# Kernel tuning notes

Hardware: AMD Instinct MI355X
Metric: run time of the kernel (lower is better)

Reference implementation:

```python
import jax, jax.numpy as jnp
import numpy as np

K = 2          # neighbors per point (init default k=2)
ALPHA = 5e-4   # regularization weight (init default)
N_CLASSES = 1000


def setup_inputs() -> dict:
    key = jax.random.key(0)
    k1, k2, k3 = jax.random.split(key, 3)
    n, d_feat, n_cls = 4096, 1024, N_CLASSES
    x_batch = jax.random.normal(k1, (n, d_feat), dtype=jnp.float32)
    y_batch = jax.random.randint(k2, (n,), 0, n_cls, dtype=jnp.int32)
    y_output = jax.random.normal(k3, (n, n_cls), dtype=jnp.float32)
    return {"x_batch": x_batch, "y_batch": y_batch, "y_output": y_output}


def _pairwise_dist(a):
    # ||a_i - a_j|| via gram trick; clamp for numerical safety.
    sq = jnp.sum(a * a, axis=-1)                       # [n]
    d2 = sq[:, None] + sq[None, :] - 2.0 * (a @ a.T)   # [n, n]
    d2 = jnp.maximum(d2, 0.0)
    # sqrt with zero-safe gradient (diag / coincident points)
    safe = jnp.where(d2 > 0.0, d2, 1.0)
    return jnp.where(d2 > 0.0, jnp.sqrt(safe), 0.0)


def reference(x_batch, y_batch, y_output):
    n = x_batch.shape[0]
    d = _pairwise_dist(x_batch)                        # [n, n] input-space distances

    # K nearest neighbors, excluding self (i != j in the original loops)
    d_knn = d + jnp.where(jnp.eye(n, dtype=bool), jnp.inf, 0.0)
    _, nbr_idx = jax.lax.top_k(-d_knn, K)              # [n, K] smallest distances
    nbr_mask = jnp.zeros((n, n), dtype=d.dtype)
    nbr_mask = nbr_mask.at[jnp.arange(n)[:, None], nbr_idx].set(1.0)

    same_class = (y_batch[:, None] == y_batch[None, :])
    w = jnp.exp(-d) * nbr_mask                         # exp(-d) on KNN edges only
    # w_diff = w_int - w_pen: +exp(-d) for same-class neighbors, -exp(-d) otherwise
    w_diff = jnp.where(same_class, w, -w)

    y_norm = _pairwise_dist(y_output)                  # [n, n] ||y_out_i - y_out_j||
    reg_value = jnp.sum(w_diff * y_norm)
    return ALPHA * reg_value
```

## Files before the change

kernel.cpp:

```cpp
#include <hip/hip_runtime.h>
#include <math.h>

#define ALPHA 5e-4f
#define BIG 1e30f

typedef __attribute__((ext_vector_type(8))) short bf16x8;
typedef __attribute__((ext_vector_type(4))) float f32x4;

__device__ __forceinline__ unsigned short f2bf(float x) {
    unsigned u = __builtin_bit_cast(unsigned, x);
    unsigned r = (u + 0x7FFFu + ((u >> 16) & 1u)) >> 16;
    return (unsigned short)r;
}
__device__ __forceinline__ float bf2f(unsigned short b) {
    unsigned u = ((unsigned)b) << 16;
    return __builtin_bit_cast(float, u);
}

__device__ __forceinline__ void gload16(const short* g, short* l) {
    __builtin_amdgcn_global_load_lds(
        (const __attribute__((address_space(1))) void*)g,
        (__attribute__((address_space(3))) void*)l, 16, 0, 0);
}

__global__ __launch_bounds__(256)
void conv_rownorm_kernel(const float* __restrict__ X, short* __restrict__ Xb,
                         float* __restrict__ sqn, int d) {
    const int w = threadIdx.x >> 6, lane = threadIdx.x & 63;
    const int row = blockIdx.x * 4 + w;
    const float4* src = reinterpret_cast<const float4*>(X + (size_t)row * d);
    short4* dst = reinterpret_cast<short4*>(Xb + (size_t)row * d);
    float s = 0.f;
    const int nv = d >> 2;
    for (int c = lane; c < nv; c += 64) {
        float4 v = src[c];
        unsigned short b0 = f2bf(v.x), b1 = f2bf(v.y), b2 = f2bf(v.z), b3 = f2bf(v.w);
        float x0 = bf2f(b0), x1 = bf2f(b1), x2 = bf2f(b2), x3 = bf2f(b3);
        s += x0 * x0 + x1 * x1 + x2 * x2 + x3 * x3;
        dst[c] = make_short4((short)b0, (short)b1, (short)b2, (short)b3);
    }
    for (int off = 1; off < 64; off <<= 1) s += __shfl_xor(s, off, 64);
    if (lane == 0) sqn[row] = s;
}

#define BM 128
#define BN 128
#define BK 32

__global__ __launch_bounds__(256)
void gram_top2_mfma(const short* __restrict__ Xb, const float* __restrict__ sqn,
                    float* __restrict__ cand_s, int* __restrict__ cand_i,
                    int n, int d, int nb) {
    __shared__ short As[2][BM * BK];
    __shared__ short Bs[2][BN * BK];

    int rb = 0, rem = blockIdx.x;
    while (rem >= nb - rb) { rem -= nb - rb; ++rb; }
    const int cb = rb + rem;

    const int row0 = rb * BM, col0 = cb * BN;
    const int t = threadIdx.x;
    const int w = t >> 6, l = t & 63;
    const int wr = w >> 1, wc = w & 1;
    const int lc = l & 15, lg = l >> 4;

    f32x4 acc[4][4];
#pragma unroll
    for (int i = 0; i < 4; ++i)
#pragma unroll
        for (int j = 0; j < 4; ++j) acc[i][j] = (f32x4){0.f, 0.f, 0.f, 0.f};

    const int gchunk = (t & 3) ^ ((t >> 3) & 3);
    const size_t gA0 = (size_t)(row0 + (t >> 2)) * d + gchunk * 8;
    const size_t gB0 = (size_t)(col0 + (t >> 2)) * d + gchunk * 8;
    const size_t rstep = (size_t)64 * d;

    const int kswz = (lg ^ ((lc >> 1) & 3)) * 8;

    {
        short* la = As[0] + w * 512;
        short* lb = Bs[0] + w * 512;
        gload16(Xb + gA0, la);
        gload16(Xb + gA0 + rstep, la + 2048);
        gload16(Xb + gB0, lb);
        gload16(Xb + gB0 + rstep, lb + 2048);
    }
    __syncthreads();

    int cur = 0;
    for (int k0 = 0; k0 < d; k0 += BK) {
        if (k0 + BK < d) {
            short* la = As[cur ^ 1] + w * 512;
            short* lb = Bs[cur ^ 1] + w * 512;
            gload16(Xb + gA0 + k0 + BK, la);
            gload16(Xb + gA0 + k0 + BK + rstep, la + 2048);
            gload16(Xb + gB0 + k0 + BK, lb);
            gload16(Xb + gB0 + k0 + BK + rstep, lb + 2048);
        }
        bf16x8 a[4], b[4];
#pragma unroll
        for (int mi = 0; mi < 4; ++mi)
            a[mi] = *reinterpret_cast<const bf16x8*>(&As[cur][(wr * 64 + mi * 16 + lc) * BK + kswz]);
#pragma unroll
        for (int ni = 0; ni < 4; ++ni)
            b[ni] = *reinterpret_cast<const bf16x8*>(&Bs[cur][(wc * 64 + ni * 16 + lc) * BK + kswz]);
#pragma unroll
        for (int mi = 0; mi < 4; ++mi)
#pragma unroll
            for (int ni = 0; ni < 4; ++ni)
                acc[mi][ni] = __builtin_amdgcn_mfma_f32_16x16x32_bf16(
                    a[mi], b[ni], acc[mi][ni], 0, 0, 0);
        __syncthreads();
        cur ^= 1;
    }

    float sq_c[4];
#pragma unroll
    for (int ni = 0; ni < 4; ++ni) sq_c[ni] = sqn[col0 + wc * 64 + ni * 16 + lc];
    const int strip_r = cb * 2 + wc;

#pragma unroll
    for (int mi = 0; mi < 4; ++mi) {
#pragma unroll
        for (int j = 0; j < 4; ++j) {
            const int grow = row0 + wr * 64 + mi * 16 + lg * 4 + j;
            float s1 = BIG, s2 = BIG;
            int i1 = -1, i2 = -1;
#pragma unroll
            for (int ni = 0; ni < 4; ++ni) {
                const int gcol = col0 + wc * 64 + ni * 16 + lc;
                float s = sq_c[ni] - 2.f * acc[mi][ni][j];
                if (gcol == grow) s = BIG;
                if (s < s1) { s2 = s1; i2 = i1; s1 = s; i1 = gcol; }
                else if (s < s2) { s2 = s; i2 = gcol; }
            }
            for (int off = 1; off < 16; off <<= 1) {
                float b1 = __shfl_xor(s1, off, 16);
                int  bi1 = __shfl_xor(i1, off, 16);
                float b2 = __shfl_xor(s2, off, 16);
                int  bi2 = __shfl_xor(i2, off, 16);
                if (b1 < s1) { s2 = s1; i2 = i1; s1 = b1; i1 = bi1; }
                else if (b1 < s2) { s2 = b1; i2 = bi1; }
                if (b2 < s2) { s2 = b2; i2 = bi2; }
            }
            if (lc == 0) {
                size_t base = ((size_t)grow * 64 + strip_r) * 2;
                cand_s[base] = s1; cand_s[base + 1] = s2;
                cand_i[base] = i1; cand_i[base + 1] = i2;
            }
        }
    }

    if (rb != cb) {
        float sq_r[4][4];
#pragma unroll
        for (int mi = 0; mi < 4; ++mi)
#pragma unroll
            for (int j = 0; j < 4; ++j)
                sq_r[mi][j] = sqn[row0 + wr * 64 + mi * 16 + lg * 4 + j];
        const int strip_c = rb * 2 + wr;

#pragma unroll
        for (int ni = 0; ni < 4; ++ni) {
            const int gcol = col0 + wc * 64 + ni * 16 + lc;
            float s1 = BIG, s2 = BIG;
            int i1 = -1, i2 = -1;
#pragma unroll
            for (int mi = 0; mi < 4; ++mi)
#pragma unroll
                for (int j = 0; j < 4; ++j) {
                    const int grow = row0 + wr * 64 + mi * 16 + lg * 4 + j;
                    float s = sq_r[mi][j] - 2.f * acc[mi][ni][j];
                    if (s < s1) { s2 = s1; i2 = i1; s1 = s; i1 = grow; }
                    else if (s < s2) { s2 = s; i2 = grow; }
                }
#pragma unroll
            for (int off = 16; off < 64; off <<= 1) {
                float b1 = __shfl_xor(s1, off, 64);
                int  bi1 = __shfl_xor(i1, off, 64);
                float b2 = __shfl_xor(s2, off, 64);
                int  bi2 = __shfl_xor(i2, off, 64);
                if (b1 < s1) { s2 = s1; i2 = i1; s1 = b1; i1 = bi1; }
                else if (b1 < s2) { s2 = b1; i2 = bi1; }
                if (b2 < s2) { s2 = b2; i2 = bi2; }
            }
            if (lg == 0) {
                size_t base = ((size_t)gcol * 64 + strip_c) * 2;
                cand_s[base] = s1; cand_s[base + 1] = s2;
                cand_i[base] = i1; cand_i[base + 1] = i2;
            }
        }
    }
}

__global__ __launch_bounds__(256)
void merge_edges_kernel(const float* __restrict__ sqn,
                        const float* __restrict__ cand_s, const int* __restrict__ cand_i,
                        const int* __restrict__ yb, const float* __restrict__ yo,
                        float* __restrict__ partial, int ncls) {
    const int w = threadIdx.x >> 6, lane = threadIdx.x & 63;
    const int row = blockIdx.x * 4 + w;

    float2 cs = reinterpret_cast<const float2*>(cand_s + (size_t)row * 128)[lane];
    int2   ci = reinterpret_cast<const int2*>(cand_i + (size_t)row * 128)[lane];
    float s1 = cs.x, s2 = cs.y;
    int i1 = ci.x, i2 = ci.y;
    if (s2 < s1) { float ts = s1; s1 = s2; s2 = ts; int ti = i1; i1 = i2; i2 = ti; }

    for (int off = 1; off < 64; off <<= 1) {
        float b1 = __shfl_xor(s1, off, 64);
        int  bi1 = __shfl_xor(i1, off, 64);
        float b2 = __shfl_xor(s2, off, 64);
        int  bi2 = __shfl_xor(i2, off, 64);
        if (b1 < s1) { s2 = s1; i2 = i1; s1 = b1; i1 = bi1; }
        else if (b1 < s2) { s2 = b1; i2 = bi1; }
        if (b2 < s2) { s2 = b2; i2 = bi2; }
    }
    const int yr = yb[row];
    const float sr = sqn[row];
    float w1 = ((yr == yb[i1]) ? 1.f : -1.f) * expf(-sqrtf(fmaxf(sr + s1, 0.f)));
    float w2 = ((yr == yb[i2]) ? 1.f : -1.f) * expf(-sqrtf(fmaxf(sr + s2, 0.f)));

    const float4* yr4 = reinterpret_cast<const float4*>(yo + (size_t)row * ncls);
    const float4* y14 = reinterpret_cast<const float4*>(yo + (size_t)i1 * ncls);
    const float4* y24 = reinterpret_cast<const float4*>(yo + (size_t)i2 * ncls);
    const int nv4 = ncls >> 2;
    float a1 = 0.f, a2 = 0.f;
    for (int c = lane; c < nv4; c += 64) {
        float4 v = yr4[c];
        float4 u1 = y14[c];
        float4 u2 = y24[c];
        float tx = v.x - u1.x, ty = v.y - u1.y, tz = v.z - u1.z, tw = v.w - u1.w;
        a1 = fmaf(tx, tx, fmaf(ty, ty, fmaf(tz, tz, fmaf(tw, tw, a1))));
        tx = v.x - u2.x; ty = v.y - u2.y; tz = v.z - u2.z; tw = v.w - u2.w;
        a2 = fmaf(tx, tx, fmaf(ty, ty, fmaf(tz, tz, fmaf(tw, tw, a2))));
    }
    for (int c = (nv4 << 2) + lane; c < ncls; c += 64) {
        float v = yo[(size_t)row * ncls + c];
        float t1 = v - yo[(size_t)i1 * ncls + c];
        float t2 = v - yo[(size_t)i2 * ncls + c];
        a1 = fmaf(t1, t1, a1);
        a2 = fmaf(t2, t2, a2);
    }
    for (int off = 1; off < 64; off <<= 1) {
        a1 += __shfl_xor(a1, off, 64);
        a2 += __shfl_xor(a2, off, 64);
    }
    if (lane == 0)
        partial[row] = w1 * sqrtf(a1) + w2 * sqrtf(a2);
}

__global__ __launch_bounds__(256)
void final_reduce_kernel(const float* __restrict__ partial, float* __restrict__ out, int n) {
    const int t = threadIdx.x;
    __shared__ float red[4];
    float s = 0.f;
    const int nv4 = n >> 2;
    const float4* p4 = reinterpret_cast<const float4*>(partial);
    for (int c = t; c < nv4; c += 256) {
        float4 v = p4[c];
        s += v.x + v.y + v.z + v.w;
    }
    for (int off = 1; off < 64; off <<= 1) s += __shfl_xor(s, off, 64);
    if ((t & 63) == 0) red[t >> 6] = s;
    __syncthreads();
    if (t == 0) out[0] = ALPHA * (red[0] + red[1] + red[2] + red[3]);
}

extern "C" void kernel_launch(void* const* d_in, const int* in_sizes, int n_in,
                              void* d_out, int out_size, void* d_ws, size_t ws_size,
                              hipStream_t stream) {
    const float* X  = (const float*)d_in[0];
    const int*   yb = (const int*)d_in[1];
    const float* yo = (const float*)d_in[2];
    float* out = (float*)d_out;

    const int n    = in_sizes[1];
    const int d    = in_sizes[0] / n;
    const int ncls = in_sizes[2] / n;
    const int nb   = n / BM;

    char* wsb = (char*)d_ws;
    size_t off = 0;
    float* sqn = (float*)(wsb + off);    off += ((size_t)n * 4 + 255) & ~(size_t)255;
    short* Xb  = (short*)(wsb + off);    off += ((size_t)n * d * 2 + 255) & ~(size_t)255;
    float* cand_s = (float*)(wsb + off); off += ((size_t)n * 64 * 2 * 4 + 255) & ~(size_t)255;
    int*   cand_i = (int*)(wsb + off);   off += ((size_t)n * 64 * 2 * 4 + 255) & ~(size_t)255;
    float* partial = (float*)(wsb + off);

    conv_rownorm_kernel<<<n / 4, 256, 0, stream>>>(X, Xb, sqn, d);

    const int ntri = nb * (nb + 1) / 2;
    gram_top2_mfma<<<ntri, 256, 0, stream>>>(Xb, sqn, cand_s, cand_i, n, d, nb);

    merge_edges_kernel<<<n / 4, 256, 0, stream>>>(sqn, cand_s, cand_i, yb, yo, partial, ncls);

    final_reduce_kernel<<<1, 256, 0, stream>>>(partial, out, n);
}
```

Before: 60.80 us.

## Triple-buffer the gram GEMM pipeline and swizzle tiles across XCDs

```diff
diff --git a/kernel.cpp b/kernel.cpp
--- a/kernel.cpp
+++ b/kernel.cpp
@@ -50,11 +50,15 @@
 __global__ __launch_bounds__(256)
 void gram_top2_mfma(const short* __restrict__ Xb, const float* __restrict__ sqn,
                     float* __restrict__ cand_s, int* __restrict__ cand_i,
-                    int n, int d, int nb) {
-    __shared__ short As[2][BM * BK];
-    __shared__ short Bs[2][BN * BK];
-
-    int rb = 0, rem = blockIdx.x;
+                    int n, int d, int nb, int cpx) {
+    __shared__ short As[3][BM * BK];
+    __shared__ short Bs[3][BN * BK];
+
+    const int nwg = nb * (nb + 1) / 2;
+    int bid = blockIdx.x;
+    int swz = (bid & 7) * cpx + (bid >> 3);
+    (void)nwg;
+    int rb = 0, rem = swz;
     while (rem >= nb - rb) { rem -= nb - rb; ++rb; }
     const int cb = rb + rem;
 
@@ -74,44 +78,52 @@
     const size_t gA0 = (size_t)(row0 + (t >> 2)) * d + gchunk * 8;
     const size_t gB0 = (size_t)(col0 + (t >> 2)) * d + gchunk * 8;
     const size_t rstep = (size_t)64 * d;
-
     const int kswz = (lg ^ ((lc >> 1) & 3)) * 8;
+    const int wbase = w * 512;
+
+    const int nsteps = d / BK;
 
     {
-        short* la = As[0] + w * 512;
-        short* lb = Bs[0] + w * 512;
-        gload16(Xb + gA0, la);
-        gload16(Xb + gA0 + rstep, la + 2048);
-        gload16(Xb + gB0, lb);
-        gload16(Xb + gB0 + rstep, lb + 2048);
-    }
-    __syncthreads();
-
-    int cur = 0;
-    for (int k0 = 0; k0 < d; k0 += BK) {
-        if (k0 + BK < d) {
-            short* la = As[cur ^ 1] + w * 512;
-            short* lb = Bs[cur ^ 1] + w * 512;
-            gload16(Xb + gA0 + k0 + BK, la);
-            gload16(Xb + gA0 + k0 + BK + rstep, la + 2048);
-            gload16(Xb + gB0 + k0 + BK, lb);
-            gload16(Xb + gB0 + k0 + BK + rstep, lb + 2048);
+        short* la = As[0] + wbase;  short* lb = Bs[0] + wbase;
+        gload16(Xb + gA0, la);          gload16(Xb + gA0 + rstep, la + 2048);
+        gload16(Xb + gB0, lb);          gload16(Xb + gB0 + rstep, lb + 2048);
+        la = As[1] + wbase;  lb = Bs[1] + wbase;
+        gload16(Xb + gA0 + BK, la);     gload16(Xb + gA0 + BK + rstep, la + 2048);
+        gload16(Xb + gB0 + BK, lb);     gload16(Xb + gB0 + BK + rstep, lb + 2048);
+    }
+
+    int s0 = 0, s1 = 1, s2 = 2;
+    for (int ks = 0; ks < nsteps; ++ks) {
+        if (ks + 2 < nsteps) {
+            short* la = As[s2] + wbase;  short* lb = Bs[s2] + wbase;
+            const size_t ko = (size_t)(ks + 2) * BK;
+            gload16(Xb + gA0 + ko, la);      gload16(Xb + gA0 + ko + rstep, la + 2048);
+            gload16(Xb + gB0 + ko, lb);      gload16(Xb + gB0 + ko + rstep, lb + 2048);
+            asm volatile("s_waitcnt vmcnt(8)" ::: "memory");
+        } else if (ks + 1 < nsteps) {
+            asm volatile("s_waitcnt vmcnt(4)" ::: "memory");
+        } else {
+            asm volatile("s_waitcnt vmcnt(0)" ::: "memory");
         }
+        __builtin_amdgcn_s_barrier();
+
         bf16x8 a[4], b[4];
 #pragma unroll
         for (int mi = 0; mi < 4; ++mi)
-            a[mi] = *reinterpret_cast<const bf16x8*>(&As[cur][(wr * 64 + mi * 16 + lc) * BK + kswz]);
+            a[mi] = *reinterpret_cast<const bf16x8*>(&As[s0][(wr * 64 + mi * 16 + lc) * BK + kswz]);
 #pragma unroll
         for (int ni = 0; ni < 4; ++ni)
-            b[ni] = *reinterpret_cast<const bf16x8*>(&Bs[cur][(wc * 64 + ni * 16 + lc) * BK + kswz]);
+            b[ni] = *reinterpret_cast<const bf16x8*>(&Bs[s0][(wc * 64 + ni * 16 + lc) * BK + kswz]);
 #pragma unroll
         for (int mi = 0; mi < 4; ++mi)
 #pragma unroll
             for (int ni = 0; ni < 4; ++ni)
                 acc[mi][ni] = __builtin_amdgcn_mfma_f32_16x16x32_bf16(
                     a[mi], b[ni], acc[mi][ni], 0, 0, 0);
-        __syncthreads();
-        cur ^= 1;
+
+        asm volatile("s_waitcnt lgkmcnt(0)" ::: "memory");
+        __builtin_amdgcn_s_barrier();
+        int tmp = s0; s0 = s1; s1 = s2; s2 = tmp;
     }
 
     float sq_c[4];
@@ -124,28 +136,28 @@
 #pragma unroll
         for (int j = 0; j < 4; ++j) {
             const int grow = row0 + wr * 64 + mi * 16 + lg * 4 + j;
-            float s1 = BIG, s2 = BIG;
+            float s1v = BIG, s2v = BIG;
             int i1 = -1, i2 = -1;
 #pragma unroll
             for (int ni = 0; ni < 4; ++ni) {
                 const int gcol = col0 + wc * 64 + ni * 16 + lc;
                 float s = sq_c[ni] - 2.f * acc[mi][ni][j];
                 if (gcol == grow) s = BIG;
-                if (s < s1) { s2 = s1; i2 = i1; s1 = s; i1 = gcol; }
-                else if (s < s2) { s2 = s; i2 = gcol; }
+                if (s < s1v) { s2v = s1v; i2 = i1; s1v = s; i1 = gcol; }
+                else if (s < s2v) { s2v = s; i2 = gcol; }
             }
             for (int off = 1; off < 16; off <<= 1) {
-                float b1 = __shfl_xor(s1, off, 16);
+                float b1 = __shfl_xor(s1v, off, 16);
                 int  bi1 = __shfl_xor(i1, off, 16);
-                float b2 = __shfl_xor(s2, off, 16);
+                float b2 = __shfl_xor(s2v, off, 16);
                 int  bi2 = __shfl_xor(i2, off, 16);
-                if (b1 < s1) { s2 = s1; i2 = i1; s1 = b1; i1 = bi1; }
-                else if (b1 < s2) { s2 = b1; i2 = bi1; }
-                if (b2 < s2) { s2 = b2; i2 = bi2; }
+                if (b1 < s1v) { s2v = s1v; i2 = i1; s1v = b1; i1 = bi1; }
+                else if (b1 < s2v) { s2v = b1; i2 = bi1; }
+                if (b2 < s2v) { s2v = b2; i2 = bi2; }
             }
             if (lc == 0) {
                 size_t base = ((size_t)grow * 64 + strip_r) * 2;
-                cand_s[base] = s1; cand_s[base + 1] = s2;
+                cand_s[base] = s1v; cand_s[base + 1] = s2v;
                 cand_i[base] = i1; cand_i[base + 1] = i2;
             }
         }
@@ -163,7 +175,7 @@
 #pragma unroll
         for (int ni = 0; ni < 4; ++ni) {
             const int gcol = col0 + wc * 64 + ni * 16 + lc;
-            float s1 = BIG, s2 = BIG;
+            float s1v = BIG, s2v = BIG;
             int i1 = -1, i2 = -1;
 #pragma unroll
             for (int mi = 0; mi < 4; ++mi)
@@ -171,22 +183,22 @@
                 for (int j = 0; j < 4; ++j) {
                     const int grow = row0 + wr * 64 + mi * 16 + lg * 4 + j;
                     float s = sq_r[mi][j] - 2.f * acc[mi][ni][j];
-                    if (s < s1) { s2 = s1; i2 = i1; s1 = s; i1 = grow; }
-                    else if (s < s2) { s2 = s; i2 = grow; }
+                    if (s < s1v) { s2v = s1v; i2 = i1; s1v = s; i1 = grow; }
+                    else if (s < s2v) { s2v = s; i2 = grow; }
                 }
 #pragma unroll
             for (int off = 16; off < 64; off <<= 1) {
-                float b1 = __shfl_xor(s1, off, 64);
+                float b1 = __shfl_xor(s1v, off, 64);
                 int  bi1 = __shfl_xor(i1, off, 64);
-                float b2 = __shfl_xor(s2, off, 64);
+                float b2 = __shfl_xor(s2v, off, 64);
                 int  bi2 = __shfl_xor(i2, off, 64);
-                if (b1 < s1) { s2 = s1; i2 = i1; s1 = b1; i1 = bi1; }
-                else if (b1 < s2) { s2 = b1; i2 = bi1; }
-                if (b2 < s2) { s2 = b2; i2 = bi2; }
+                if (b1 < s1v) { s2v = s1v; i2 = i1; s1v = b1; i1 = bi1; }
+                else if (b1 < s2v) { s2v = b1; i2 = bi1; }
+                if (b2 < s2v) { s2v = b2; i2 = bi2; }
             }
             if (lg == 0) {
                 size_t base = ((size_t)gcol * 64 + strip_c) * 2;
-                cand_s[base] = s1; cand_s[base + 1] = s2;
+                cand_s[base] = s1v; cand_s[base + 1] = s2v;
                 cand_i[base] = i1; cand_i[base + 1] = i2;
             }
         }
@@ -291,7 +303,8 @@
     conv_rownorm_kernel<<<n / 4, 256, 0, stream>>>(X, Xb, sqn, d);
 
     const int ntri = nb * (nb + 1) / 2;
-    gram_top2_mfma<<<ntri, 256, 0, stream>>>(Xb, sqn, cand_s, cand_i, n, d, nb);
+    const int cpx  = ntri / 8;
+    gram_top2_mfma<<<ntri, 256, 0, stream>>>(Xb, sqn, cand_s, cand_i, n, d, nb, cpx);
 
     merge_edges_kernel<<<n / 4, 256, 0, stream>>>(sqn, cand_s, cand_i, yb, yo, partial, ncls);
 
```

New measurement: 60.67 us. No clear change (-0.2%).
